# Kernel optimization log

Hardware: AMD Instinct MI355X
Metric: run time of the kernel (lower is better)

The kernel has to match this reference:

```python
import jax, jax.numpy as jnp
import numpy as np

M = 4       # window size
NH = 6      # num heads
EPS = 1e-5


def _layernorm(x, g, b):
    mu = jnp.mean(x, axis=-1, keepdims=True)
    var = jnp.mean(jnp.square(x - mu), axis=-1, keepdims=True)
    return (x - mu) * jax.lax.rsqrt(var + EPS) * g + b


def _window_attn(xw, wq, wk, wv, wo):
    # xw: [num_windows, L=M*M, C]
    Bw, L, C = xw.shape
    dh = C // NH
    q = (xw @ wq).reshape(Bw, L, NH, dh)
    k = (xw @ wk).reshape(Bw, L, NH, dh)
    v = (xw @ wv).reshape(Bw, L, NH, dh)
    # NOTE: original scales by hidden_dim**-0.5, not head_dim**-0.5
    scores = jnp.einsum('binh,bjnh->bnij', q, k) * (C ** -0.5)
    aw = jax.nn.softmax(scores, axis=-1)
    y = jnp.einsum('bnij,bjnh->binh', aw, v).reshape(Bw, L, C)
    return y @ wo


def setup_inputs() -> dict:
    key = jax.random.key(0)
    ks = jax.random.split(key, 8)
    B, C, H, W = 32, 192, 64, 64
    MLP_D = 768
    s = C ** -0.5
    return {
        'x':  jax.random.normal(ks[0], (B, C, H, W), jnp.float32),
        'wq': jax.random.normal(ks[1], (C, C), jnp.float32) * s,
        'wk': jax.random.normal(ks[2], (C, C), jnp.float32) * s,
        'wv': jax.random.normal(ks[3], (C, C), jnp.float32) * s,
        'wo': jax.random.normal(ks[4], (C, C), jnp.float32) * s,
        'w1': jax.random.normal(ks[5], (C, MLP_D), jnp.float32) * s,
        'b1': jnp.zeros((MLP_D,), jnp.float32),
        'w2': jax.random.normal(ks[6], (MLP_D, C), jnp.float32) * (MLP_D ** -0.5),
        'b2': jnp.zeros((C,), jnp.float32),
        'g1': jnp.ones((C,), jnp.float32),
        'beta1': jnp.zeros((C,), jnp.float32),
        'g2': jnp.ones((C,), jnp.float32),
        'beta2': jnp.zeros((C,), jnp.float32),
    }


def reference(x, wq, wk, wv, wo, w1, b1, w2, b2, g1, beta1, g2, beta2):
    B, C, H, W = x.shape
    hh, ww = H // M, W // M
    xt = jnp.transpose(x, (0, 2, 3, 1))  # [B,H,W,C]

    # window partition per 'b c (M1 h) (M2 w) -> (b h w) (M1 M2) c'
    # (window index is the OUTER factor of each spatial dim -> strided windows)
    xw = xt.reshape(B, M, hh, M, ww, C)
    xw = jnp.transpose(xw, (0, 2, 4, 1, 3, 5)).reshape(B * hh * ww, M * M, C)

    yw = _window_attn(xw, wq, wk, wv, wo)

    # merge windows back: [(b h w), (M1 M2), c] -> [B,H,W,C]
    y = yw.reshape(B, hh, ww, M, M, C)
    y = jnp.transpose(y, (0, 3, 1, 4, 2, 5)).reshape(B, H, W, C)

    # residual + LayerNorm (post-norm, as in ResidualConnection)
    x1 = _layernorm(y + xt, g1, beta1)

    # MLP (exact GELU as nn.GELU default) + residual + LayerNorm
    h = jax.nn.gelu(x1 @ w1 + b1, approximate=False)
    m = h @ w2 + b2
    x2 = _layernorm(m + x1, g2, beta2)

    return jnp.transpose(x2, (0, 3, 1, 2))  # [B,C,H,W]
```

## Files before the change

kernel.cpp:

```cpp
#include <hip/hip_runtime.h>
#include <hip/hip_bf16.h>
#include <math.h>


#define DEVI __device__ __forceinline__

static constexpr int CH   = 192;
static constexpr int NTOK = 32 * 64 * 64;
static constexpr int MLPD = 768;

typedef short bf16x8 __attribute__((ext_vector_type(8)));
typedef float f32x4  __attribute__((ext_vector_type(4)));

DEVI float bf2f(unsigned short u) { return __uint_as_float(((unsigned)u) << 16); }
DEVI unsigned short f2bf(float f) {
    __hip_bfloat16 h = __float2bfloat16(f);
    return *reinterpret_cast<unsigned short*>(&h);
}

DEVI void gload_lds16(const void* g, void* l) {
    __builtin_amdgcn_global_load_lds(
        (const __attribute__((address_space(1))) void*)g,
        (__attribute__((address_space(3))) void*)l, 16, 0, 0);
}

DEVI float gelu_f(float v) {
    float z = fabsf(v) * 0.70710678118654752f;
    float t = 1.0f / (1.0f + 0.3275911f * z);
    float poly = ((((1.061405429f * t - 1.453152027f) * t + 1.421413741f) * t
                   - 0.284496736f) * t + 0.254829592f) * t;
    float erfv = 1.0f - poly * __expf(-z * z);
    erfv = (v < 0.f) ? -erfv : erfv;
    return 0.5f * v * (1.0f + erfv);
}

__global__ __launch_bounds__(256) void k_wprep(const float* __restrict__ W,
                                               __hip_bfloat16* __restrict__ Wt,
                                               int K, int N) {
    int idx = blockIdx.x * 256 + threadIdx.x;
    if (idx >= K * N) return;
    int n = idx / K, k = idx - n * K;
    Wt[idx] = __float2bfloat16(W[(size_t)k * N + n]);
}

__global__ __launch_bounds__(256) void k_tin(const float* __restrict__ x,
                                             __hip_bfloat16* __restrict__ xt) {
    __shared__ float lds[CH * 65];
    int bh = blockIdx.x;
    int b = bh >> 6, h = bh & 63;
    const float* xp = x + ((size_t)b * CH) * 4096 + (size_t)h * 64;
    int tid = threadIdx.x;
    int w = tid & 63;
    #pragma unroll
    for (int it = 0; it < CH / 4; ++it) {
        int c = it * 4 + (tid >> 6);
        lds[c * 65 + w] = xp[(size_t)c * 4096 + w];
    }
    __syncthreads();
    int m1 = h >> 4, h0 = h & 15;
    int ubase = (b << 12) | (h0 << 8) | (m1 << 2);
    #pragma unroll
    for (int it = 0; it < 48; ++it) {
        int idx = it * 256 + tid;
        int tok = idx / CH;
        int c = idx - tok * CH;
        int u = ubase | ((tok & 15) << 4) | (tok >> 4);
        xt[(size_t)u * CH + c] = __float2bfloat16(lds[c * 65 + tok]);
    }
}

template<int K, int NCB, bool GELU, bool BIAS>
__global__ __launch_bounds__(256) void k_mgemm(const __hip_bfloat16* __restrict__ A,
                                               const __hip_bfloat16* __restrict__ Bt,
                                               const float* __restrict__ bias,
                                               __hip_bfloat16* __restrict__ Cm,
                                               const int nbase,
                                               const int LDA, const int LDC) {
    __shared__ __align__(16) char smem[24576];
    const int tid = threadIdx.x;
    const int l  = tid & 63;
    const int w  = tid >> 6;
    const int wr = w >> 1, wc = w & 1;
    const int per = (int)gridDim.x >> 3;
    const int bid = (int)blockIdx.x;
    const int swz = (bid & 7) * per + (bid >> 3);
    const int r0 = (swz / NCB) * 128;
    const int n0 = nbase + (swz % NCB) * 64;
    constexpr int NT = K / 32;

    f32x4 acc[4][2] = {};

    auto stage = [&](int bi, int kt) {
        #pragma unroll
        for (int it = 0; it < 2; ++it) {
            int c = it * 4 + w, s = c * 64 + l;
            int row = s >> 2, seg = s & 3;
            int sseg = seg ^ ((row >> 1) & 3);
            gload_lds16(A + (size_t)(r0 + row) * LDA + kt * 32 + sseg * 8,
                        smem + bi * 12288 + c * 1024);
        }
        {
            int c = w, s = c * 64 + l;
            int row = s >> 2, seg = s & 3;
            int sseg = seg ^ ((row >> 1) & 3);
            gload_lds16(Bt + (size_t)(n0 + row) * K + kt * 32 + sseg * 8,
                        smem + bi * 12288 + 8192 + c * 1024);
        }
    };

    stage(0, 0);
    __syncthreads();
    #pragma unroll
    for (int kt = 0; kt < NT; ++kt) {
        const int cur = kt & 1;
        if (kt + 1 < NT) stage(cur ^ 1, kt + 1);
        char* As = smem + cur * 12288;
        char* Bs = smem + cur * 12288 + 8192;
        const int kq = l >> 4;
        bf16x8 af[4], bfr[2];
        #pragma unroll
        for (int m = 0; m < 4; ++m) {
            int row = wr * 64 + m * 16 + (l & 15);
            af[m] = *(const bf16x8*)(As + row * 64 + ((kq ^ ((row >> 1) & 3)) << 4));
        }
        #pragma unroll
        for (int n = 0; n < 2; ++n) {
            int row = wc * 32 + n * 16 + (l & 15);
            bfr[n] = *(const bf16x8*)(Bs + row * 64 + ((kq ^ ((row >> 1) & 3)) << 4));
        }
        #pragma unroll
        for (int m = 0; m < 4; ++m)
            #pragma unroll
            for (int n = 0; n < 2; ++n)
                acc[m][n] = __builtin_amdgcn_mfma_f32_16x16x32_bf16(
                    bfr[n], af[m], acc[m][n], 0, 0, 0);
        __syncthreads();
    }

    const int cl = l & 15;
    const int kq = l >> 4;
    #pragma unroll
    for (int m = 0; m < 4; ++m) {
        size_t row = (size_t)r0 + wr * 64 + m * 16 + cl;
        #pragma unroll
        for (int n = 0; n < 2; ++n) {
            int colb = n0 + wc * 32 + n * 16 + kq * 4;
            float4 bv = make_float4(0.f, 0.f, 0.f, 0.f);
            if constexpr (BIAS) bv = *reinterpret_cast<const float4*>(bias + colb);
            union { uint2 u2; unsigned short us[4]; } pk;
            #pragma unroll
            for (int j = 0; j < 4; ++j) {
                float v = acc[m][n][j] + (&bv.x)[j];
                if constexpr (GELU) v = gelu_f(v);
                pk.us[j] = f2bf(v);
            }
            *reinterpret_cast<uint2*>(Cm + row * LDC + colb) = pk.u2;
        }
    }
}

template<int K, bool BIAS>
__global__ __launch_bounds__(256) void k_gemmln(const __hip_bfloat16* __restrict__ A,
                                                const __hip_bfloat16* __restrict__ Bt,
                                                const float* __restrict__ bias,
                                                const __hip_bfloat16* Res,
                                                const float* __restrict__ g,
                                                const float* __restrict__ be,
                                                __hip_bfloat16* Out,
                                                const int LDA) {
    __shared__ __align__(16) char smem[65536];
    const int tid = threadIdx.x;
    const int l  = tid & 63;
    const int w  = tid >> 6;
    const int cl = l & 15;
    const int kq = l >> 4;
    const int r0 = blockIdx.x * 64;
    constexpr int NT = K / 64;

    f32x4 acc[12] = {};

    auto stage = [&](int bi, int kt) {
        #pragma unroll
        for (int it = 0; it < 2; ++it) {
            int c = it * 4 + w, s = c * 64 + l, row = s >> 3;
            int eb = ((s & 7) << 4) ^ ((row & 7) << 4);
            gload_lds16(A + (size_t)(r0 + row) * LDA + kt * 64 + (eb >> 1),
                        smem + bi * 32768 + c * 1024);
        }
        #pragma unroll
        for (int it = 0; it < 6; ++it) {
            int c = it * 4 + w, s = c * 64 + l, row = s >> 3;
            int eb = ((s & 7) << 4) ^ ((row & 7) << 4);
            gload_lds16(Bt + (size_t)row * K + kt * 64 + (eb >> 1),
                        smem + bi * 32768 + 8192 + c * 1024);
        }
    };

    stage(0, 0);
    __syncthreads();
    #pragma unroll
    for (int kt = 0; kt < NT; ++kt) {
        const int cur = kt & 1;
        if (kt + 1 < NT) stage(cur ^ 1, kt + 1);
        char* As = smem + cur * 32768;
        char* Bs = smem + cur * 32768 + 8192;
        #pragma unroll
        for (int ks = 0; ks < 2; ++ks) {
            int kb = ks * 64 + (kq << 4);
            int arow = w * 16 + cl;
            bf16x8 af = *(const bf16x8*)(As + arow * 128 + (kb ^ ((arow & 7) << 4)));
            #pragma unroll
            for (int n = 0; n < 12; ++n) {
                int row = n * 16 + cl;
                bf16x8 b = *(const bf16x8*)(Bs + row * 128 + (kb ^ ((row & 7) << 4)));
                acc[n] = __builtin_amdgcn_mfma_f32_16x16x32_bf16(af, b, acc[n], 0, 0, 0);
            }
        }
        __syncthreads();
    }

    float gv[12], bev[12], bv[12];
    #pragma unroll
    for (int n = 0; n < 12; ++n) {
        int col = n * 16 + cl;
        gv[n]  = g[col];
        bev[n] = be[col];
        bv[n]  = BIAS ? bias[col] : 0.f;
    }
    #pragma unroll
    for (int r = 0; r < 4; ++r) {
        size_t row = (size_t)r0 + w * 16 + kq * 4 + r;
        float v[12];
        float sum = 0.f;
        #pragma unroll
        for (int n = 0; n < 12; ++n) {
            int col = n * 16 + cl;
            v[n] = acc[n][r] + bv[n] +
                   bf2f(*reinterpret_cast<const unsigned short*>(Res + row * 192 + col));
            sum += v[n];
        }
        sum += __shfl_xor(sum, 1);
        sum += __shfl_xor(sum, 2);
        sum += __shfl_xor(sum, 4);
        sum += __shfl_xor(sum, 8);
        float mean = sum * (1.0f / 192.0f);
        float ss = 0.f;
        #pragma unroll
        for (int n = 0; n < 12; ++n) { v[n] -= mean; ss += v[n] * v[n]; }
        ss += __shfl_xor(ss, 1);
        ss += __shfl_xor(ss, 2);
        ss += __shfl_xor(ss, 4);
        ss += __shfl_xor(ss, 8);
        float rs = rsqrtf(ss * (1.0f / 192.0f) + 1e-5f);
        #pragma unroll
        for (int n = 0; n < 12; ++n) {
            int col = n * 16 + cl;
            *reinterpret_cast<unsigned short*>(Out + row * 192 + col) =
                f2bf(v[n] * rs * gv[n] + bev[n]);
        }
    }
}

__global__ __launch_bounds__(256) void k_attn2(__hip_bfloat16* qkv) {
    __shared__ __align__(16) char lds[4 * 13568];
    const int tid = threadIdx.x;
    const int l = tid & 63;
    const int w = tid >> 6;
    const int win = blockIdx.x * 4 + w;
    char* vt = lds + w * 13568;
    char* pb = vt + 12288;

    #pragma unroll
    for (int rr = 0; rr < 3; ++rr) {
        char* zp = vt + (l * 3 + rr) * 64 + 32;
        *(uint4*)zp        = make_uint4(0u, 0u, 0u, 0u);
        *(uint4*)(zp + 16) = make_uint4(0u, 0u, 0u, 0u);
    }
    {
        int r = l >> 2, o = (l & 3) * 8;
        *(uint2*)(pb + r * 80 + 32 + o) = make_uint2(0u, 0u);
    }

    const __hip_bfloat16* base = qkv + (size_t)win * 16 * 576;

    uint4 vr[6];
    #pragma unroll
    for (int it = 0; it < 6; ++it) {
        int flat = it * 64 + l;
        int row = flat / 24, seg = flat - row * 24;
        vr[it] = *(const uint4*)(base + (size_t)row * 576 + 384 + seg * 8);
    }
    bf16x8 qf[6], kf[6];
    #pragma unroll
    for (int h = 0; h < 6; ++h) {
        const __hip_bfloat16* rp = base + (size_t)(l & 15) * 576;
        int off = h * 32 + (l >> 4) * 8;
        qf[h] = *(const bf16x8*)(rp + off);
        kf[h] = *(const bf16x8*)(rp + 192 + off);
    }
    #pragma unroll
    for (int it = 0; it < 6; ++it) {
        int flat = it * 64 + l;
        int row = flat / 24, seg = flat - row * 24;
        const unsigned short* e = (const unsigned short*)&vr[it];
        #pragma unroll
        for (int j = 0; j < 8; ++j)
            *(unsigned short*)(vt + (seg * 8 + j) * 64 + row * 2) = e[j];
    }

    const float scale = 0.07216878364870322f;
    __hip_bfloat16* yp = qkv + (size_t)win * 16 * 576 + 384;

    #pragma unroll
    for (int h = 0; h < 6; ++h) {
        f32x4 s = {};
        s = __builtin_amdgcn_mfma_f32_16x16x32_bf16(kf[h], qf[h], s, 0, 0, 0);
        float sc[4];
        #pragma unroll
        for (int r = 0; r < 4; ++r) sc[r] = s[r] * scale;
        float mx = fmaxf(fmaxf(sc[0], sc[1]), fmaxf(sc[2], sc[3]));
        mx = fmaxf(mx, __shfl_xor(mx, 16));
        mx = fmaxf(mx, __shfl_xor(mx, 32));
        float e0 = __expf(sc[0] - mx), e1 = __expf(sc[1] - mx);
        float e2 = __expf(sc[2] - mx), e3 = __expf(sc[3] - mx);
        float sum = e0 + e1 + e2 + e3;
        sum += __shfl_xor(sum, 16);
        sum += __shfl_xor(sum, 32);
        float inv = 1.0f / sum;
        unsigned int pa = ((unsigned)f2bf(e1 * inv) << 16) | f2bf(e0 * inv);
        unsigned int pc = ((unsigned)f2bf(e3 * inv) << 16) | f2bf(e2 * inv);
        char* pw = pb + (l & 15) * 80 + (l >> 4) * 8;
        *(unsigned int*)pw = pa;
        *(unsigned int*)(pw + 4) = pc;
        bf16x8 pf = *(const bf16x8*)(pb + (l & 15) * 80 + (l >> 4) * 16);
        bf16x8 v0 = *(const bf16x8*)(vt + (h * 32 + (l & 15)) * 64 + (l >> 4) * 16);
        bf16x8 v1 = *(const bf16x8*)(vt + (h * 32 + 16 + (l & 15)) * 64 + (l >> 4) * 16);
        f32x4 y0 = {}, y1 = {};
        y0 = __builtin_amdgcn_mfma_f32_16x16x32_bf16(pf, v0, y0, 0, 0, 0);
        y1 = __builtin_amdgcn_mfma_f32_16x16x32_bf16(pf, v1, y1, 0, 0, 0);
        #pragma unroll
        for (int r = 0; r < 4; ++r) {
            int row = (l >> 4) * 4 + r;
            yp[(size_t)row * 576 + h * 32 + (l & 15)]      = __float2bfloat16(y0[r]);
            yp[(size_t)row * 576 + h * 32 + 16 + (l & 15)] = __float2bfloat16(y1[r]);
        }
    }
}

__global__ __launch_bounds__(256) void k_tout(const __hip_bfloat16* __restrict__ X2,
                                              float* __restrict__ out) {
    __shared__ float lds[CH * 65];
    int bh = blockIdx.x;
    int b = bh >> 6, h = bh & 63;
    int tid = threadIdx.x;
    int m1 = h >> 4, h0 = h & 15;
    int ubase = (b << 12) | (h0 << 8) | (m1 << 2);
    #pragma unroll
    for (int it = 0; it < 12; ++it) {
        int idx = it * 256 + tid;
        int tok = idx / 48, cq = idx - tok * 48;
        int u = ubase | ((tok & 15) << 4) | (tok >> 4);
        uint2 ma = *reinterpret_cast<const uint2*>(X2 + (size_t)u * CH + cq * 4);
        const unsigned short* ms = reinterpret_cast<const unsigned short*>(&ma);
        #pragma unroll
        for (int j = 0; j < 4; ++j) lds[(cq * 4 + j) * 65 + tok] = bf2f(ms[j]);
    }
    __syncthreads();
    float* op = out + (size_t)b * CH * 4096 + (size_t)h * 64;
    #pragma unroll
    for (int it = 0; it < 48; ++it) {
        int idx = it * 256 + tid;
        int c = idx >> 6;
        int w = idx & 63;
        op[(size_t)c * 4096 + w] = lds[c * 65 + w];
    }
}

extern "C" void kernel_launch(void* const* d_in, const int* in_sizes, int n_in,
                              void* d_out, int out_size, void* d_ws, size_t ws_size,
                              hipStream_t stream) {
    const float* x   = (const float*)d_in[0];
    const float* wq  = (const float*)d_in[1];
    const float* wk  = (const float*)d_in[2];
    const float* wv  = (const float*)d_in[3];
    const float* wo  = (const float*)d_in[4];
    const float* w1  = (const float*)d_in[5];
    const float* b1  = (const float*)d_in[6];
    const float* w2  = (const float*)d_in[7];
    const float* b2  = (const float*)d_in[8];
    const float* g1  = (const float*)d_in[9];
    const float* be1 = (const float*)d_in[10];
    const float* g2  = (const float*)d_in[11];
    const float* be2 = (const float*)d_in[12];
    float* out = (float*)d_out;

    char* ws = (char*)d_ws;
    const size_t SZ = (size_t)NTOK * CH * sizeof(__hip_bfloat16);
    __hip_bfloat16* xt   = (__hip_bfloat16*)(ws);
    __hip_bfloat16* qkv  = (__hip_bfloat16*)(ws + SZ);
    __hip_bfloat16* x1   = xt;
    __hip_bfloat16* hb   = qkv;

    __hip_bfloat16* wqkvt = (__hip_bfloat16*)(ws + 4 * SZ);
    __hip_bfloat16* wot   = wqkvt + 576 * 192;
    __hip_bfloat16* w1t   = wot + 192 * 192;
    __hip_bfloat16* w2t   = w1t + 192 * 768;

    k_wprep<<<144, 256, 0, stream>>>(wq, wqkvt,             192, 192);
    k_wprep<<<144, 256, 0, stream>>>(wk, wqkvt + 192 * 192, 192, 192);
    k_wprep<<<144, 256, 0, stream>>>(wv, wqkvt + 384 * 192, 192, 192);
    k_wprep<<<144, 256, 0, stream>>>(wo, wot, 192, 192);
    k_wprep<<<576, 256, 0, stream>>>(w1, w1t, 192, 768);
    k_wprep<<<576, 256, 0, stream>>>(w2, w2t, 768, 192);

    k_tin<<<2048, 256, 0, stream>>>(x, xt);

    k_mgemm<192, 9, false, false><<<9216, 256, 0, stream>>>(
        xt, wqkvt, nullptr, qkv, 0, 192, 576);
    k_attn2<<<NTOK / 64, 256, 0, stream>>>(qkv);
    k_gemmln<192, false><<<NTOK / 64, 256, 0, stream>>>(
        qkv + 384, wot, nullptr, xt, g1, be1, x1, 576);

    const int CHUNK = 65536;
    for (int c = 0; c < 2; ++c) {
        __hip_bfloat16* x1c = x1 + (size_t)c * CHUNK * CH;
        k_mgemm<192, 12, true, true><<<6144, 256, 0, stream>>>(
            x1c, w1t, b1, hb, 0, 192, MLPD);
        k_gemmln<768, true><<<CHUNK / 64, 256, 0, stream>>>(
            hb, w2t, b2, x1c, g2, be2, x1c, MLPD);
    }
    k_tout<<<2048, 256, 0, stream>>>(x1, out);
}
```

Measured before the change: 414.6 us.

## Load full-K A tile into LDS once and keep B fragments in registers

The generic GEMM used for QKV and MLP-up projections now stages the whole 128x192 A tile into LDS in one pass with an XOR swizzle. It loads all of the B (weight) fragments directly from global memory into registers, replacing the double-buffered per-32-K pipeline with its per-iteration barriers. This removes five barriers and the B LDS traffic. In exchange it raises LDS use to 48KB and adds register pressure, which may reduce occupancy, and there is no longer any overlap of loads with compute within a block.

Result: slower. 469.7 us (+13.3%).

```diff
diff --git a/kernel.cpp b/kernel.cpp
--- a/kernel.cpp
+++ b/kernel.cpp
@@ -69,14 +69,15 @@
     }
 }
 
-template<int K, int NCB, bool GELU, bool BIAS>
+template<int NCB, bool GELU, bool BIAS>
 __global__ __launch_bounds__(256) void k_mgemm(const __hip_bfloat16* __restrict__ A,
                                                const __hip_bfloat16* __restrict__ Bt,
                                                const float* __restrict__ bias,
                                                __hip_bfloat16* __restrict__ Cm,
                                                const int nbase,
                                                const int LDA, const int LDC) {
-    __shared__ __align__(16) char smem[24576];
+    constexpr int K = 192;
+    __shared__ __align__(16) char Als[49152];
     const int tid = threadIdx.x;
     const int l  = tid & 63;
     const int w  = tid >> 6;
@@ -86,59 +87,45 @@
     const int swz = (bid & 7) * per + (bid >> 3);
     const int r0 = (swz / NCB) * 128;
     const int n0 = nbase + (swz % NCB) * 64;
-    constexpr int NT = K / 32;
+    const int cl = l & 15;
+    const int kq = l >> 4;
+
+    #pragma unroll
+    for (int it = 0; it < 12; ++it) {
+        int c = it * 4 + w;
+        int s = c * 64 + l;
+        int row = s / 24, cc = s - row * 24;
+        gload_lds16(A + (size_t)(r0 + row) * LDA + (cc ^ (row & 7)) * 8,
+                    Als + c * 1024);
+    }
+    bf16x8 bfr[6][2];
+    #pragma unroll
+    for (int kt = 0; kt < 6; ++kt)
+        #pragma unroll
+        for (int n = 0; n < 2; ++n) {
+            int row = wc * 32 + n * 16 + cl;
+            bfr[kt][n] = *(const bf16x8*)(Bt + (size_t)(n0 + row) * K + kt * 32 + kq * 8);
+        }
+    __syncthreads();
 
     f32x4 acc[4][2] = {};
-
-    auto stage = [&](int bi, int kt) {
-        #pragma unroll
-        for (int it = 0; it < 2; ++it) {
-            int c = it * 4 + w, s = c * 64 + l;
-            int row = s >> 2, seg = s & 3;
-            int sseg = seg ^ ((row >> 1) & 3);
-            gload_lds16(A + (size_t)(r0 + row) * LDA + kt * 32 + sseg * 8,
-                        smem + bi * 12288 + c * 1024);
-        }
-        {
-            int c = w, s = c * 64 + l;
-            int row = s >> 2, seg = s & 3;
-            int sseg = seg ^ ((row >> 1) & 3);
-            gload_lds16(Bt + (size_t)(n0 + row) * K + kt * 32 + sseg * 8,
-                        smem + bi * 12288 + 8192 + c * 1024);
-        }
-    };
-
-    stage(0, 0);
-    __syncthreads();
-    #pragma unroll
-    for (int kt = 0; kt < NT; ++kt) {
-        const int cur = kt & 1;
-        if (kt + 1 < NT) stage(cur ^ 1, kt + 1);
-        char* As = smem + cur * 12288;
-        char* Bs = smem + cur * 12288 + 8192;
-        const int kq = l >> 4;
-        bf16x8 af[4], bfr[2];
+    #pragma unroll
+    for (int kt = 0; kt < 6; ++kt) {
+        bf16x8 af[4];
         #pragma unroll
         for (int m = 0; m < 4; ++m) {
-            int row = wr * 64 + m * 16 + (l & 15);
-            af[m] = *(const bf16x8*)(As + row * 64 + ((kq ^ ((row >> 1) & 3)) << 4));
-        }
-        #pragma unroll
-        for (int n = 0; n < 2; ++n) {
-            int row = wc * 32 + n * 16 + (l & 15);
-            bfr[n] = *(const bf16x8*)(Bs + row * 64 + ((kq ^ ((row >> 1) & 3)) << 4));
+            int row = wr * 64 + m * 16 + cl;
+            int cc = kt * 4 + kq;
+            af[m] = *(const bf16x8*)(Als + row * 384 + ((cc ^ (row & 7)) << 4));
         }
         #pragma unroll
         for (int m = 0; m < 4; ++m)
             #pragma unroll
             for (int n = 0; n < 2; ++n)
                 acc[m][n] = __builtin_amdgcn_mfma_f32_16x16x32_bf16(
-                    bfr[n], af[m], acc[m][n], 0, 0, 0);
-        __syncthreads();
-    }
-
-    const int cl = l & 15;
-    const int kq = l >> 4;
+                    bfr[kt][n], af[m], acc[m][n], 0, 0, 0);
+    }
+
     #pragma unroll
     for (int m = 0; m < 4; ++m) {
         size_t row = (size_t)r0 + wr * 64 + m * 16 + cl;
@@ -415,7 +402,7 @@
 
     k_tin<<<2048, 256, 0, stream>>>(x, xt);
 
-    k_mgemm<192, 9, false, false><<<9216, 256, 0, stream>>>(
+    k_mgemm<9, false, false><<<9216, 256, 0, stream>>>(
         xt, wqkvt, nullptr, qkv, 0, 192, 576);
     k_attn2<<<NTOK / 64, 256, 0, stream>>>(qkv);
     k_gemmln<192, false><<<NTOK / 64, 256, 0, stream>>>(
@@ -424,7 +411,7 @@
     const int CHUNK = 65536;
     for (int c = 0; c < 2; ++c) {
         __hip_bfloat16* x1c = x1 + (size_t)c * CHUNK * CH;
-        k_mgemm<192, 12, true, true><<<6144, 256, 0, stream>>>(
+        k_mgemm<12, true, true><<<6144, 256, 0, stream>>>(
             x1c, w1t, b1, hb, 0, 192, MLPD);
         k_gemmln<768, true><<<CHUNK / 64, 256, 0, stream>>>(
             hb, w2t, b2, x1c, g2, be2, x1c, MLPD);
```
